# Optimization experiments

Hardware: AMD Instinct MI355X
Metric: run time of the kernel (lower is better)

The kernel has to match this reference:

```python
import jax, jax.numpy as jnp
import numpy as np

D_MODEL = 768
NHEAD = 12
HEAD_DIM = D_MODEL // NHEAD
WINDOW = 33  # band half-width = 16


def setup_inputs() -> dict:
    key = jax.random.key(0)
    ks = jax.random.split(key, 9)
    B, T, C = 2, 4096, D_MODEL
    s = 0.02
    return {
        "x": jax.random.normal(ks[0], (B, T, C), jnp.float32),
        "Wq": jax.random.normal(ks[1], (C, C), jnp.float32) * s,
        "bq": jnp.zeros((C,), jnp.float32),
        "Wk": jax.random.normal(ks[2], (C, C), jnp.float32) * s,
        "bk": jnp.zeros((C,), jnp.float32),
        "Wv": jax.random.normal(ks[3], (C, C), jnp.float32) * s,
        "bv": jnp.zeros((C,), jnp.float32),
        "Wo": jax.random.normal(ks[4], (C, C), jnp.float32) * s,
        "bo": jnp.zeros((C,), jnp.float32),
    }


def reference(x, Wq, bq, Wk, bk, Wv, bv, Wo, bo):
    B, T, C = x.shape
    H, D = NHEAD, HEAD_DIM
    scale = D ** -0.5
    # torch Linear: x @ W.T + b
    q = (x @ Wq.T + bq).reshape(B, T, H, D).transpose(0, 2, 1, 3)  # [B,H,T,D]
    k = (x @ Wk.T + bk).reshape(B, T, H, D).transpose(0, 2, 1, 3)
    v = (x @ Wv.T + bv).reshape(B, T, H, D).transpose(0, 2, 1, 3)
    scores = jnp.einsum("bhqd,bhkd->bhqk", q, k) * scale  # [B,H,T,T]
    idx = jnp.arange(T)
    local_mask = jnp.abs(idx[:, None] - idx[None, :]) <= (WINDOW // 2)  # [T,T]
    scores = jnp.where(local_mask[None, None], scores, -jnp.inf)
    attn = jax.nn.softmax(scores, axis=-1)  # dropout=0 / eval mode
    out = jnp.einsum("bhqk,bhkd->bhqd", attn, v)  # [B,H,T,D]
    out = out.transpose(0, 2, 1, 3).reshape(B, T, C)
    return out @ Wo.T + bo
```

## Files before the change

### kernel.cpp

```cpp
#include <hip/hip_runtime.h>
#include <math.h>
#include <cstdint>
#include <cstddef>

typedef unsigned short u16;
typedef short bf16x8 __attribute__((ext_vector_type(8)));
typedef float f32x4 __attribute__((ext_vector_type(4)));
typedef u16 u16x8 __attribute__((ext_vector_type(8)));
typedef u16 u16x4 __attribute__((ext_vector_type(4)));

#define T_LEN 4096
#define NH 12
#define HD 64
#define DMODEL 768
#define GK 768
#define QKV_STRIDE 6291456ul

__device__ __forceinline__ u16 f2bf(float x) {
  union { float f; unsigned u; } v; v.f = x;
  unsigned r = v.u + 0x7fffu + ((v.u >> 16) & 1u);
  return (u16)(r >> 16);
}
__device__ __forceinline__ float bf2f(u16 x) {
  union { unsigned u; float f; } v; v.u = ((unsigned)x) << 16;
  return v.f;
}
__device__ __forceinline__ void bfpair(unsigned u, float& lo, float& hi) {
  union { unsigned u; float f; } a, b;
  a.u = u << 16; b.u = u & 0xffff0000u;
  lo = a.f; hi = b.f;
}

__device__ __forceinline__ void async16(const u16* g, u16* l) {
  __builtin_amdgcn_global_load_lds(
      (const __attribute__((address_space(1))) unsigned int*)g,
      (__attribute__((address_space(3))) unsigned int*)l, 16, 0, 0);
}

__global__ void cvt_f32_bf16(const float* __restrict__ s, u16* __restrict__ d, int n) {
  int i = (blockIdx.x * blockDim.x + threadIdx.x) * 4;
  if (i >= n) return;
  float4 v = *(const float4*)(s + i);
  u16x4 o;
  o[0] = f2bf(v.x); o[1] = f2bf(v.y); o[2] = f2bf(v.z); o[3] = f2bf(v.w);
  *(u16x4*)(d + i) = o;
}

__global__ void cvt_w4(const float* __restrict__ s0, const float* __restrict__ s1,
                       const float* __restrict__ s2, const float* __restrict__ s3,
                       u16* __restrict__ d0, u16* __restrict__ d1,
                       u16* __restrict__ d2, u16* __restrict__ d3) {
  const float* s; u16* d;
  switch (blockIdx.y) {
    case 0: s = s0; d = d0; break;
    case 1: s = s1; d = d1; break;
    case 2: s = s2; d = d2; break;
    default: s = s3; d = d3; break;
  }
  int i = (blockIdx.x * blockDim.x + threadIdx.x) * 4;
  float4 v = *(const float4*)(s + i);
  u16x4 o;
  o[0] = f2bf(v.x); o[1] = f2bf(v.y); o[2] = f2bf(v.z); o[3] = f2bf(v.w);
  *(u16x4*)(d + i) = o;
}

#define BM 128
#define BN 128
#define BK 32

template <int EPI>
__global__ __launch_bounds__(256)
void gemm_bt(const u16* __restrict__ A, const u16* __restrict__ B,
             const float* __restrict__ bias0, const float* __restrict__ bias1,
             const float* __restrict__ bias2, void* __restrict__ outp) {
  extern __shared__ __align__(16) u16 smem[];
  u16* As = smem;
  u16* Bs = smem + BM * BK;
  u16* Cs = smem + (BM + BN) * BK;

  const int tid  = threadIdx.x;
  const int lane = tid & 63;
  const int wave = tid >> 6;
  const int wm = wave & 1, wn = wave >> 1;
  const long am0 = (long)blockIdx.x * BM;
  const long bn0 = (long)blockIdx.y * BN;
  const int r16 = lane & 15;
  const int kh  = lane >> 4;
  const int sw8 = (kh ^ ((r16 >> 1) & 3)) * 8;

  f32x4 acc[4][4] = {};

  const int srow   = lane >> 2;
  const int schunk = ((lane & 3) ^ ((lane >> 3) & 3)) * 8;
  const u16* Ag = A + (am0 + wave * 16 + srow) * GK + schunk;
  const u16* Bg = B + (bn0 + wave * 16 + srow) * GK + schunk;
  u16* Al0 = &As[(wave * 16) * BK];
  u16* Al1 = &As[(64 + wave * 16) * BK];
  u16* Bl0 = &Bs[(wave * 16) * BK];
  u16* Bl1 = &Bs[(64 + wave * 16) * BK];

  for (int kt = 0; kt < GK; kt += BK) {
    __syncthreads();
    async16(Ag + kt, Al0);
    async16(Ag + 64 * GK + kt, Al1);
    async16(Bg + kt, Bl0);
    async16(Bg + 64 * GK + kt, Bl1);
    __syncthreads();
    bf16x8 af[4], bfr[4];
#pragma unroll
    for (int i = 0; i < 4; i++)
      af[i] = *(const bf16x8*)&As[(wm * 64 + i * 16 + r16) * BK + sw8];
#pragma unroll
    for (int j = 0; j < 4; j++)
      bfr[j] = *(const bf16x8*)&Bs[(wn * 64 + j * 16 + r16) * BK + sw8];
#pragma unroll
    for (int i = 0; i < 4; i++)
#pragma unroll
      for (int j = 0; j < 4; j++)
        acc[i][j] = __builtin_amdgcn_mfma_f32_16x16x32_bf16(af[i], bfr[j], acc[i][j], 0, 0, 0);
  }

  const int m0 = (int)am0 + wm * 64;
  const int n0w = wn * 64;

  if (EPI == 0) {
    const int tens = (int)(bn0 >= 1536 ? 2 : (bn0 >= 768 ? 1 : 0));
    const int c0 = (int)bn0 - tens * 768;
    const float* bp = (tens == 0) ? bias0 : ((tens == 1) ? bias1 : bias2);
    u16* outb = (u16*)outp + (size_t)tens * QKV_STRIDE;

#pragma unroll
    for (int j = 0; j < 4; j++) {
      float bv = bp[c0 + n0w + j * 16 + r16];
      int lc = n0w + j * 16 + r16;
#pragma unroll
      for (int i = 0; i < 4; i++) {
        int lr = wm * 64 + i * 16 + kh * 4;
#pragma unroll
        for (int r = 0; r < 4; r++)
          Cs[(lr + r) * BN + lc] = f2bf(acc[i][j][r] + bv);
      }
    }
    __syncthreads();
#pragma unroll
    for (int z = 0; z < 8; z++) {
      int cidx = z * 256 + tid;
      int row = cidx >> 4, ch = (cidx & 15) * 8;
      uint4 val = *(const uint4*)&Cs[row * BN + ch];
      *(uint4*)(outb + (size_t)(am0 + row) * DMODEL + c0 + ch) = val;
    }
  } else {
    float* O = (float*)outp;
#pragma unroll
    for (int i = 0; i < 4; i++) {
#pragma unroll
      for (int r = 0; r < 4; r++) {
        int row = m0 + i * 16 + kh * 4 + r;
        float* orow = O + (size_t)row * DMODEL;
#pragma unroll
        for (int j = 0; j < 4; j++) {
          int col = (int)bn0 + n0w + j * 16 + r16;
          orow[col] = acc[i][j][r] + bias0[col];
        }
      }
    }
  }
}

#define QB 64
#define SLAB 96
#define KSTR 72

__global__ __launch_bounds__(256)
void attn_local(const u16* __restrict__ qkv, u16* __restrict__ attn) {
  __shared__ __align__(16) u16 Ks[SLAB][KSTR];
  __shared__ __align__(16) u16 Vs[SLAB][KSTR];
  const int tid = threadIdx.x;
  const int q0 = blockIdx.x * QB;
  const int h = blockIdx.y, b = blockIdx.z;
  const size_t rowbase = (size_t)b * T_LEN;
  const int hc = h * HD;
  const u16* Qg = qkv;
  const u16* Kg = qkv + QKV_STRIDE;
  const u16* Vg = qkv + 2 * QKV_STRIDE;

  for (int e = tid; e < SLAB * 8; e += 256) {
    int r = e >> 3, c8 = (e & 7) * 8;
    int g = q0 - 16 + r;
    if (g >= 0 && g < T_LEN) {
      size_t off = (rowbase + g) * DMODEL + hc + c8;
      *(u16x8*)&Ks[r][c8] = *(const u16x8*)(Kg + off);
      *(u16x8*)&Vs[r][c8] = *(const u16x8*)(Vg + off);
    } else {
      u16x8 zz = {0, 0, 0, 0, 0, 0, 0, 0};
      *(u16x8*)&Ks[r][c8] = zz;
      *(u16x8*)&Vs[r][c8] = zz;
    }
  }

  const int qi = tid >> 2;
  const int p  = tid & 3;
  const int d0 = p * 16;
  const int t  = q0 + qi;

  float qv[16];
  {
    const u16* qrow = Qg + (rowbase + t) * DMODEL + hc + d0;
    uint4 a = *(const uint4*)qrow;
    uint4 bq = *(const uint4*)(qrow + 8);
    bfpair(a.x, qv[0], qv[1]);   bfpair(a.y, qv[2], qv[3]);
    bfpair(a.z, qv[4], qv[5]);   bfpair(a.w, qv[6], qv[7]);
    bfpair(bq.x, qv[8], qv[9]);  bfpair(bq.y, qv[10], qv[11]);
    bfpair(bq.z, qv[12], qv[13]); bfpair(bq.w, qv[14], qv[15]);
  }
  __syncthreads();

  float s[33];
#pragma unroll
  for (int j = 0; j < 33; j++) {
    const int row = qi + j;
    uint4 a = *(const uint4*)&Ks[row][d0];
    uint4 c = *(const uint4*)&Ks[row][d0 + 8];
    float k0, k1;
    float a0 = 0.f, a1 = 0.f;
    bfpair(a.x, k0, k1); a0 += qv[0] * k0;  a1 += qv[1] * k1;
    bfpair(a.y, k0, k1); a0 += qv[2] * k0;  a1 += qv[3] * k1;
    bfpair(a.z, k0, k1); a0 += qv[4] * k0;  a1 += qv[5] * k1;
    bfpair(a.w, k0, k1); a0 += qv[6] * k0;  a1 += qv[7] * k1;
    bfpair(c.x, k0, k1); a0 += qv[8] * k0;  a1 += qv[9] * k1;
    bfpair(c.y, k0, k1); a0 += qv[10] * k0; a1 += qv[11] * k1;
    bfpair(c.z, k0, k1); a0 += qv[12] * k0; a1 += qv[13] * k1;
    bfpair(c.w, k0, k1); a0 += qv[14] * k0; a1 += qv[15] * k1;
    float sc = a0 + a1;
    sc += __shfl_xor(sc, 1);
    sc += __shfl_xor(sc, 2);
    int kidx = t - 16 + j;
    s[j] = (kidx >= 0 && kidx < T_LEN) ? sc * 0.125f : -INFINITY;
  }

  float m = s[0];
#pragma unroll
  for (int j = 1; j < 33; j++) m = fmaxf(m, s[j]);
  float l = 0.f;
#pragma unroll
  for (int j = 0; j < 33; j++) {
    float pp = __expf(s[j] - m);
    s[j] = pp;
    l += pp;
  }
  float inv = 1.0f / l;

  float o[16] = {};
#pragma unroll
  for (int j = 0; j < 33; j++) {
    const int row = qi + j;
    float pp = s[j];
    uint4 a = *(const uint4*)&Vs[row][d0];
    uint4 c = *(const uint4*)&Vs[row][d0 + 8];
    float v0, v1;
    bfpair(a.x, v0, v1); o[0]  += pp * v0; o[1]  += pp * v1;
    bfpair(a.y, v0, v1); o[2]  += pp * v0; o[3]  += pp * v1;
    bfpair(a.z, v0, v1); o[4]  += pp * v0; o[5]  += pp * v1;
    bfpair(a.w, v0, v1); o[6]  += pp * v0; o[7]  += pp * v1;
    bfpair(c.x, v0, v1); o[8]  += pp * v0; o[9]  += pp * v1;
    bfpair(c.y, v0, v1); o[10] += pp * v0; o[11] += pp * v1;
    bfpair(c.z, v0, v1); o[12] += pp * v0; o[13] += pp * v1;
    bfpair(c.w, v0, v1); o[14] += pp * v0; o[15] += pp * v1;
  }

  u16* orow = attn + (rowbase + t) * DMODEL + hc + d0;
  u16x8 ov;
#pragma unroll
  for (int z = 0; z < 8; z++) ov[z] = f2bf(o[z] * inv);
  *(u16x8*)orow = ov;
#pragma unroll
  for (int z = 0; z < 8; z++) ov[z] = f2bf(o[8 + z] * inv);
  *(u16x8*)(orow + 8) = ov;
}

extern "C" void kernel_launch(void* const* d_in, const int* in_sizes, int n_in,
                              void* d_out, int out_size, void* d_ws, size_t ws_size,
                              hipStream_t stream) {
  const float* x  = (const float*)d_in[0];
  const float* Wq = (const float*)d_in[1];
  const float* bq = (const float*)d_in[2];
  const float* Wk = (const float*)d_in[3];
  const float* bk = (const float*)d_in[4];
  const float* Wv = (const float*)d_in[5];
  const float* bv = (const float*)d_in[6];
  const float* Wo = (const float*)d_in[7];
  const float* bo = (const float*)d_in[8];
  float* out = (float*)d_out;
  char* ws = (char*)d_ws;

  u16* xb   = (u16*)(ws);
  u16* wqkv = (u16*)(ws + 12582912);
  u16* wo_b = (u16*)(ws + 16121856);
  u16* qkv  = (u16*)(ws + 17301504);
  u16* attn = (u16*)(ws + 55050240);

  cvt_f32_bf16<<<6144, 256, 0, stream>>>(x, xb, 6291456);
  cvt_w4<<<dim3(576, 4), 256, 0, stream>>>(Wq, Wk, Wv, Wo,
                                           wqkv, wqkv + 589824, wqkv + 1179648, wo_b);

  gemm_bt<0><<<dim3(64, 18), 256, 49152, stream>>>(xb, wqkv, bq, bk, bv, (void*)qkv);
  attn_local<<<dim3(64, 12, 2), 256, 0, stream>>>(qkv, attn);
  gemm_bt<1><<<dim3(64, 6), 256, 16384, stream>>>(attn, wo_b, bo, bo, bo, (void*)out);
}
```

Baseline: 187.6 us.

## Merge conversion kernels, drop LDS epilogue staging, halve output GEMM tile rows

Folds the two f32-to-bf16 conversion launches into one kernel, which saves a launch. The QKV GEMM epilogue no longer stages results through shared memory and instead writes bf16 directly from registers; this frees 32KB of LDS but makes the global stores 2-byte and scattered. The output projection GEMM is templated to 64-row tiles, doubling its grid from 384 to 768 blocks to fill more CUs. Shared memory becomes statically sized.

After: 187.3 us. About the same (-0.1%).

```diff
diff --git a/kernel.cpp b/kernel.cpp
--- a/kernel.cpp
+++ b/kernel.cpp
@@ -37,129 +37,108 @@
       (__attribute__((address_space(3))) unsigned int*)l, 16, 0, 0);
 }
 
-__global__ void cvt_f32_bf16(const float* __restrict__ s, u16* __restrict__ d, int n) {
-  int i = (blockIdx.x * blockDim.x + threadIdx.x) * 4;
-  if (i >= n) return;
+__global__ void cvt_all(const float* __restrict__ x,
+                        const float* __restrict__ Wq, const float* __restrict__ Wk,
+                        const float* __restrict__ Wv, const float* __restrict__ Wo,
+                        u16* __restrict__ xb, u16* __restrict__ wqkv, u16* __restrict__ wo_b) {
+  int bx = blockIdx.x;
+  const float* s; u16* d; int base;
+  if (bx < 6144)      { s = x;  d = xb;             base = bx; }
+  else if (bx < 6720) { s = Wq; d = wqkv;           base = bx - 6144; }
+  else if (bx < 7296) { s = Wk; d = wqkv + 589824;  base = bx - 6720; }
+  else if (bx < 7872) { s = Wv; d = wqkv + 1179648; base = bx - 7296; }
+  else                { s = Wo; d = wo_b;           base = bx - 7872; }
+  int i = (base * 256 + (int)threadIdx.x) * 4;
   float4 v = *(const float4*)(s + i);
   u16x4 o;
   o[0] = f2bf(v.x); o[1] = f2bf(v.y); o[2] = f2bf(v.z); o[3] = f2bf(v.w);
   *(u16x4*)(d + i) = o;
 }
 
-__global__ void cvt_w4(const float* __restrict__ s0, const float* __restrict__ s1,
-                       const float* __restrict__ s2, const float* __restrict__ s3,
-                       u16* __restrict__ d0, u16* __restrict__ d1,
-                       u16* __restrict__ d2, u16* __restrict__ d3) {
-  const float* s; u16* d;
-  switch (blockIdx.y) {
-    case 0: s = s0; d = d0; break;
-    case 1: s = s1; d = d1; break;
-    case 2: s = s2; d = d2; break;
-    default: s = s3; d = d3; break;
-  }
-  int i = (blockIdx.x * blockDim.x + threadIdx.x) * 4;
-  float4 v = *(const float4*)(s + i);
-  u16x4 o;
-  o[0] = f2bf(v.x); o[1] = f2bf(v.y); o[2] = f2bf(v.z); o[3] = f2bf(v.w);
-  *(u16x4*)(d + i) = o;
-}
-
-#define BM 128
 #define BN 128
 #define BK 32
 
-template <int EPI>
+template <int EPI, int MI>
 __global__ __launch_bounds__(256)
 void gemm_bt(const u16* __restrict__ A, const u16* __restrict__ B,
              const float* __restrict__ bias0, const float* __restrict__ bias1,
              const float* __restrict__ bias2, void* __restrict__ outp) {
-  extern __shared__ __align__(16) u16 smem[];
-  u16* As = smem;
-  u16* Bs = smem + BM * BK;
-  u16* Cs = smem + (BM + BN) * BK;
+  constexpr int BMt = MI * 32;
+  __shared__ __align__(16) u16 As[BMt * BK];
+  __shared__ __align__(16) u16 Bs[BN * BK];
 
   const int tid  = threadIdx.x;
   const int lane = tid & 63;
   const int wave = tid >> 6;
   const int wm = wave & 1, wn = wave >> 1;
-  const long am0 = (long)blockIdx.x * BM;
+  const long am0 = (long)blockIdx.x * BMt;
   const long bn0 = (long)blockIdx.y * BN;
   const int r16 = lane & 15;
   const int kh  = lane >> 4;
   const int sw8 = (kh ^ ((r16 >> 1) & 3)) * 8;
 
-  f32x4 acc[4][4] = {};
+  f32x4 acc[MI][4] = {};
 
   const int srow   = lane >> 2;
   const int schunk = ((lane & 3) ^ ((lane >> 3) & 3)) * 8;
   const u16* Ag = A + (am0 + wave * 16 + srow) * GK + schunk;
   const u16* Bg = B + (bn0 + wave * 16 + srow) * GK + schunk;
-  u16* Al0 = &As[(wave * 16) * BK];
-  u16* Al1 = &As[(64 + wave * 16) * BK];
   u16* Bl0 = &Bs[(wave * 16) * BK];
   u16* Bl1 = &Bs[(64 + wave * 16) * BK];
 
   for (int kt = 0; kt < GK; kt += BK) {
     __syncthreads();
-    async16(Ag + kt, Al0);
-    async16(Ag + 64 * GK + kt, Al1);
+#pragma unroll
+    for (int s = 0; s < MI / 2; s++)
+      async16(Ag + (size_t)(s * 64) * GK + kt, &As[(s * 64 + wave * 16) * BK]);
     async16(Bg + kt, Bl0);
     async16(Bg + 64 * GK + kt, Bl1);
     __syncthreads();
-    bf16x8 af[4], bfr[4];
-#pragma unroll
-    for (int i = 0; i < 4; i++)
-      af[i] = *(const bf16x8*)&As[(wm * 64 + i * 16 + r16) * BK + sw8];
+    bf16x8 af[MI], bfr[4];
+#pragma unroll
+    for (int i = 0; i < MI; i++)
+      af[i] = *(const bf16x8*)&As[(wm * MI * 16 + i * 16 + r16) * BK + sw8];
 #pragma unroll
     for (int j = 0; j < 4; j++)
       bfr[j] = *(const bf16x8*)&Bs[(wn * 64 + j * 16 + r16) * BK + sw8];
 #pragma unroll
-    for (int i = 0; i < 4; i++)
+    for (int i = 0; i < MI; i++)
 #pragma unroll
       for (int j = 0; j < 4; j++)
         acc[i][j] = __builtin_amdgcn_mfma_f32_16x16x32_bf16(af[i], bfr[j], acc[i][j], 0, 0, 0);
   }
 
-  const int m0 = (int)am0 + wm * 64;
-  const int n0w = wn * 64;
+  const int m0 = (int)am0 + wm * MI * 16;
 
   if (EPI == 0) {
-    const int tens = (int)(bn0 >= 1536 ? 2 : (bn0 >= 768 ? 1 : 0));
+    const int tens = (int)(bn0 / 768);
     const int c0 = (int)bn0 - tens * 768;
     const float* bp = (tens == 0) ? bias0 : ((tens == 1) ? bias1 : bias2);
     u16* outb = (u16*)outp + (size_t)tens * QKV_STRIDE;
-
 #pragma unroll
     for (int j = 0; j < 4; j++) {
-      float bv = bp[c0 + n0w + j * 16 + r16];
-      int lc = n0w + j * 16 + r16;
-#pragma unroll
-      for (int i = 0; i < 4; i++) {
-        int lr = wm * 64 + i * 16 + kh * 4;
-#pragma unroll
-        for (int r = 0; r < 4; r++)
-          Cs[(lr + r) * BN + lc] = f2bf(acc[i][j][r] + bv);
+      int col = c0 + wn * 64 + j * 16 + r16;
+      float bv = bp[col];
+#pragma unroll
+      for (int i = 0; i < MI; i++) {
+#pragma unroll
+        for (int r = 0; r < 4; r++) {
+          int row = m0 + i * 16 + kh * 4 + r;
+          outb[(size_t)row * DMODEL + col] = f2bf(acc[i][j][r] + bv);
+        }
       }
-    }
-    __syncthreads();
-#pragma unroll
-    for (int z = 0; z < 8; z++) {
-      int cidx = z * 256 + tid;
-      int row = cidx >> 4, ch = (cidx & 15) * 8;
-      uint4 val = *(const uint4*)&Cs[row * BN + ch];
-      *(uint4*)(outb + (size_t)(am0 + row) * DMODEL + c0 + ch) = val;
     }
   } else {
     float* O = (float*)outp;
 #pragma unroll
-    for (int i = 0; i < 4; i++) {
+    for (int i = 0; i < MI; i++) {
 #pragma unroll
       for (int r = 0; r < 4; r++) {
         int row = m0 + i * 16 + kh * 4 + r;
         float* orow = O + (size_t)row * DMODEL;
 #pragma unroll
         for (int j = 0; j < 4; j++) {
-          int col = (int)bn0 + n0w + j * 16 + r16;
+          int col = (int)bn0 + wn * 64 + j * 16 + r16;
           orow[col] = acc[i][j][r] + bias0[col];
         }
       }
@@ -299,11 +278,9 @@
   u16* qkv  = (u16*)(ws + 17301504);
   u16* attn = (u16*)(ws + 55050240);
 
-  cvt_f32_bf16<<<6144, 256, 0, stream>>>(x, xb, 6291456);
-  cvt_w4<<<dim3(576, 4), 256, 0, stream>>>(Wq, Wk, Wv, Wo,
-                                           wqkv, wqkv + 589824, wqkv + 1179648, wo_b);
-
-  gemm_bt<0><<<dim3(64, 18), 256, 49152, stream>>>(xb, wqkv, bq, bk, bv, (void*)qkv);
+  cvt_all<<<8448, 256, 0, stream>>>(x, Wq, Wk, Wv, Wo, xb, wqkv, wo_b);
+
+  gemm_bt<0, 4><<<dim3(64, 18), 256, 0, stream>>>(xb, wqkv, bq, bk, bv, (void*)qkv);
   attn_local<<<dim3(64, 12, 2), 256, 0, stream>>>(qkv, attn);
-  gemm_bt<1><<<dim3(64, 6), 256, 16384, stream>>>(attn, wo_b, bo, bo, bo, (void*)out);
-}
+  gemm_bt<1, 2><<<dim3(128, 6), 256, 0, stream>>>(attn, wo_b, bo, bo, bo, (void*)out);
+}
```
